# Kernel tuning notes

Measured on AMD Instinct MI355X. Metric: run time of the kernel, lower is better.

## Reference

```python
import jax, jax.numpy as jnp
import numpy as np

N = 8192


def setup_inputs() -> dict:
    key = jax.random.key(0)
    k1, k2 = jax.random.split(key)
    # dense symmetric-style weight matrix (adjacency/Laplacian analog)
    info_mtx = jax.random.uniform(k1, (N, N), dtype=jnp.float32)
    state = jax.random.normal(k2, (N,), dtype=jnp.float32)
    return {"info_mtx": info_mtx, "state": state}


def reference(info_mtx, state):
    # pb_type == 'maxcut': G = -0.5 * info_mtx
    G = -0.5 * info_mtx
    # Original python loop: sum over i<=j of G[i,j]*s_i*s_j (diag term linear in s_i)
    offdiag = jnp.triu(G, k=1)                     # strictly upper triangle [N,N]
    diag = jnp.diagonal(G)                         # [N]
    quad = jnp.dot(state, offdiag @ state)         # sum_{i<j} G_ij s_i s_j
    lin = jnp.dot(diag, state)                     # sum_i G_ii s_i
    total = -(quad + lin)
    num_edges = jnp.sum(info_mtx) / 2.0
    return num_edges / 2.0 - total
```

## Files before the change

### kernel.cpp

```cpp
#include <hip/hip_runtime.h>


static constexpr int N_DIM       = 8192;
static constexpr int VEC_PER_ROW = N_DIM / 4;
static constexpr int TOTAL_VEC   = N_DIM * VEC_PER_ROW;
static constexpr int BLOCK       = 256;
static constexpr int GRID        = 8192;

__global__ __launch_bounds__(BLOCK) void ising_partial_kernel(
    const float4* __restrict__ mtx4,
    const float*  __restrict__ state,
    float*        __restrict__ partial)
{
    const int tid    = blockIdx.x * BLOCK + threadIdx.x;
    const int stride = GRID * BLOCK;
    const float4* state4 = (const float4*)state;

    float acc = 0.0f;
    for (int v = tid; v < TOTAL_VEC; v += stride) {
        const int row = v >> 11;
        const int t   = v & 2047;
        const int j0  = t << 2;

        const float4 m  = mtx4[v];
        const float4 sj = state4[t];
        const float  si = state[row];

        acc += 0.25f * ((m.x + m.y) + (m.z + m.w));

        float c;
        c  = (j0 + 0 > row) ? (sj.x * m.x) : ((j0 + 0 == row) ? m.x : 0.0f);
        c += (j0 + 1 > row) ? (sj.y * m.y) : ((j0 + 1 == row) ? m.y : 0.0f);
        c += (j0 + 2 > row) ? (sj.z * m.z) : ((j0 + 2 == row) ? m.z : 0.0f);
        c += (j0 + 3 > row) ? (sj.w * m.w) : ((j0 + 3 == row) ? m.w : 0.0f);
        acc -= 0.5f * si * c;
    }

    for (int off = 32; off > 0; off >>= 1)
        acc += __shfl_down(acc, off, 64);

    __shared__ float lds[BLOCK / 64];
    const int lane = threadIdx.x & 63;
    const int wave = threadIdx.x >> 6;
    if (lane == 0) lds[wave] = acc;
    __syncthreads();
    if (threadIdx.x == 0)
        partial[blockIdx.x] = (lds[0] + lds[1]) + (lds[2] + lds[3]);
}

__global__ __launch_bounds__(BLOCK) void ising_final_kernel(
    const float* __restrict__ partial,
    float*       __restrict__ out)
{
    float acc = 0.0f;
    for (int i = threadIdx.x; i < GRID; i += BLOCK)
        acc += partial[i];

    for (int off = 32; off > 0; off >>= 1)
        acc += __shfl_down(acc, off, 64);

    __shared__ float lds[BLOCK / 64];
    const int lane = threadIdx.x & 63;
    const int wave = threadIdx.x >> 6;
    if (lane == 0) lds[wave] = acc;
    __syncthreads();
    if (threadIdx.x == 0)
        out[0] = (lds[0] + lds[1]) + (lds[2] + lds[3]);
}

extern "C" void kernel_launch(void* const* d_in, const int* in_sizes, int n_in,
                              void* d_out, int out_size, void* d_ws, size_t ws_size,
                              hipStream_t stream) {
    const float* mtx   = (const float*)d_in[0];
    const float* state = (const float*)d_in[1];
    float* out     = (float*)d_out;
    float* partial = (float*)d_ws;

    ising_partial_kernel<<<GRID, BLOCK, 0, stream>>>((const float4*)mtx, state, partial);
    ising_final_kernel<<<1, BLOCK, 0, stream>>>(partial, out);
}
```

Baseline: 360.1 us.

## Map one block per row, skip state loads below diagonal, preload row

Restructures the partial kernel so each block handles one matrix row, loading all eight float4 per thread up front for memory-level parallelism. The state vector is read only for the upper-triangular part, and the per-element row/column index math and selects are removed except on the diagonal vector. The row scale is hoisted out, FMAs replace separate multiply-adds, and the final reduction uses a wider block. The kernel stays bound by streaming the 256 MB matrix, so compute and state-load savings may matter little.

```diff
diff --git a/kernel.cpp b/kernel.cpp
--- a/kernel.cpp
+++ b/kernel.cpp
@@ -1,40 +1,57 @@
 #include <hip/hip_runtime.h>
 
 
-static constexpr int N_DIM       = 8192;
-static constexpr int VEC_PER_ROW = N_DIM / 4;
-static constexpr int TOTAL_VEC   = N_DIM * VEC_PER_ROW;
-static constexpr int BLOCK       = 256;
-static constexpr int GRID        = 8192;
+static constexpr int N_DIM = 8192;
+static constexpr int VPR   = N_DIM / 4;
+static constexpr int BLOCK = 256;
+static constexpr int ITERS = VPR / BLOCK;
+static constexpr int FBLOCK = 1024;
 
-__global__ __launch_bounds__(BLOCK) void ising_partial_kernel(
+__global__ __launch_bounds__(BLOCK) void ising_row_kernel(
     const float4* __restrict__ mtx4,
     const float*  __restrict__ state,
     float*        __restrict__ partial)
 {
-    const int tid    = blockIdx.x * BLOCK + threadIdx.x;
-    const int stride = GRID * BLOCK;
-    const float4* state4 = (const float4*)state;
+    const int   row = blockIdx.x;
+    const int   d   = row >> 2;
+    const float p   = -0.5f * state[row];
+    const float4* __restrict__ rowp = mtx4 + (size_t)row * VPR;
+    const float4* __restrict__ s4   = (const float4*)state;
 
-    float acc = 0.0f;
-    for (int v = tid; v < TOTAL_VEC; v += stride) {
-        const int row = v >> 11;
-        const int t   = v & 2047;
-        const int j0  = t << 2;
+    float4 m[ITERS];
+#pragma unroll
+    for (int k = 0; k < ITERS; ++k)
+        m[k] = rowp[threadIdx.x + (k << 8)];
 
-        const float4 m  = mtx4[v];
-        const float4 sj = state4[t];
-        const float  si = state[row];
+    float accA = 0.0f;
+    float accQ = 0.0f;
+#pragma unroll
+    for (int k = 0; k < ITERS; ++k) {
+        const int    v  = threadIdx.x + (k << 8);
+        const float4 mm = m[k];
+        accA += (mm.x + mm.y) + (mm.z + mm.w);
+        if (v > d) {
+            const float4 sj = s4[v];
+            accQ = fmaf(mm.x, sj.x, accQ);
+            accQ = fmaf(mm.y, sj.y, accQ);
+            accQ = fmaf(mm.z, sj.z, accQ);
+            accQ = fmaf(mm.w, sj.w, accQ);
+        } else if (v == d) {
+            const float4 sj = s4[v];
+            const int j0 = v << 2;
+            float w;
+            w = (j0 + 0 > row) ? sj.x : ((j0 + 0 == row) ? 1.0f : 0.0f);
+            accQ = fmaf(mm.x, w, accQ);
+            w = (j0 + 1 > row) ? sj.y : ((j0 + 1 == row) ? 1.0f : 0.0f);
+            accQ = fmaf(mm.y, w, accQ);
+            w = (j0 + 2 > row) ? sj.z : ((j0 + 2 == row) ? 1.0f : 0.0f);
+            accQ = fmaf(mm.z, w, accQ);
+            w = (j0 + 3 > row) ? sj.w : ((j0 + 3 == row) ? 1.0f : 0.0f);
+            accQ = fmaf(mm.w, w, accQ);
+        }
+    }
 
-        acc += 0.25f * ((m.x + m.y) + (m.z + m.w));
-
-        float c;
-        c  = (j0 + 0 > row) ? (sj.x * m.x) : ((j0 + 0 == row) ? m.x : 0.0f);
-        c += (j0 + 1 > row) ? (sj.y * m.y) : ((j0 + 1 == row) ? m.y : 0.0f);
-        c += (j0 + 2 > row) ? (sj.z * m.z) : ((j0 + 2 == row) ? m.z : 0.0f);
-        c += (j0 + 3 > row) ? (sj.w * m.w) : ((j0 + 3 == row) ? m.w : 0.0f);
-        acc -= 0.5f * si * c;
-    }
+    float acc = fmaf(0.25f, accA, p * accQ);
 
     for (int off = 32; off > 0; off >>= 1)
         acc += __shfl_down(acc, off, 64);
@@ -48,24 +65,29 @@
         partial[blockIdx.x] = (lds[0] + lds[1]) + (lds[2] + lds[3]);
 }
 
-__global__ __launch_bounds__(BLOCK) void ising_final_kernel(
+__global__ __launch_bounds__(FBLOCK) void ising_final_kernel(
     const float* __restrict__ partial,
     float*       __restrict__ out)
 {
     float acc = 0.0f;
-    for (int i = threadIdx.x; i < GRID; i += BLOCK)
-        acc += partial[i];
+#pragma unroll
+    for (int k = 0; k < N_DIM / FBLOCK; ++k)
+        acc += partial[threadIdx.x + k * FBLOCK];
 
     for (int off = 32; off > 0; off >>= 1)
         acc += __shfl_down(acc, off, 64);
 
-    __shared__ float lds[BLOCK / 64];
+    __shared__ float lds[FBLOCK / 64];
     const int lane = threadIdx.x & 63;
     const int wave = threadIdx.x >> 6;
     if (lane == 0) lds[wave] = acc;
     __syncthreads();
-    if (threadIdx.x == 0)
-        out[0] = (lds[0] + lds[1]) + (lds[2] + lds[3]);
+    if (threadIdx.x == 0) {
+        float s = 0.0f;
+#pragma unroll
+        for (int w = 0; w < FBLOCK / 64; ++w) s += lds[w];
+        out[0] = s;
+    }
 }
 
 extern "C" void kernel_launch(void* const* d_in, const int* in_sizes, int n_in,
@@ -76,6 +98,6 @@
     float* out     = (float*)d_out;
     float* partial = (float*)d_ws;
 
-    ising_partial_kernel<<<GRID, BLOCK, 0, stream>>>((const float4*)mtx, state, partial);
-    ising_final_kernel<<<1, BLOCK, 0, stream>>>(partial, out);
+    ising_row_kernel<<<N_DIM, BLOCK, 0, stream>>>((const float4*)mtx, state, partial);
+    ising_final_kernel<<<1, FBLOCK, 0, stream>>>(partial, out);
 }
```

New measurement: 351.4 us. -2.4%, faster.
